# Kernel optimization log

Hardware: AMD Instinct MI355X
Metric: run time of the kernel (lower is better)

## Reference

```python
import jax, jax.numpy as jnp
import numpy as np

L_LEVELS = 10
LEVEL_DIM = 4
BASE_RES = 16
T_HASH = 2 ** 21
DEG_VIEW = 4
DENSITY_BIAS = -1.0
RGB_PADDING = 0.001
RES = (BASE_RES * 2 ** np.arange(L_LEVELS)).astype(np.float32)  # 16..8192
CORNERS = np.array([[(i >> 2) & 1, (i >> 1) & 1, i & 1] for i in range(8)], np.int32)  # [8,3]
P1 = jnp.uint32(2654435761)
P2 = jnp.uint32(805459861)


def hash_grid_encode(pts, embeddings):
    """pts [N,3] in [-1,1]; embeddings [L,T,D] -> [N,L,D] trilinear hash-grid features."""
    x01 = (pts + 1.0) * 0.5  # [N,3] in [0,1]

    def level(emb, r):
        pos = x01 * r - 0.5  # align_corners=False style
        p0 = jnp.floor(pos)
        frac = pos - p0  # [N,3]
        coords = (p0.astype(jnp.int32)[:, None, :] + CORNERS).astype(jnp.uint32)  # [N,8,3]
        h = coords[..., 0] ^ (coords[..., 1] * P1) ^ (coords[..., 2] * P2)
        idx = (h & jnp.uint32(T_HASH - 1)).astype(jnp.int32)  # [N,8]
        w = jnp.prod(jnp.where(CORNERS == 1, frac[:, None, :], 1.0 - frac[:, None, :]), axis=-1)  # [N,8]
        vals = emb[idx]  # [N,8,D]
        return jnp.einsum('ncd,nc->nd', vals, w)

    feats = jax.vmap(level)(embeddings, jnp.asarray(RES))  # [L,N,D]
    return jnp.moveaxis(feats, 0, 1)  # [N,L,D]


def pos_enc(d, min_deg=0, max_deg=DEG_VIEW):
    scales = 2.0 ** jnp.arange(min_deg, max_deg, dtype=jnp.float32)
    xb = (d[..., None, :] * scales[:, None]).reshape(*d.shape[:-1], -1)  # [...,3*deg]
    four = jnp.sin(jnp.concatenate([xb, xb + 0.5 * jnp.pi], axis=-1))
    return jnp.concatenate([d, four], axis=-1)  # [..., 3 + 6*deg] = 27


def setup_inputs() -> dict:
    key = jax.random.key(0)
    ks = jax.random.split(key, 10)
    B, S, n = 1024, 32, 6
    means = jax.random.uniform(ks[0], (B, S, n, 3), minval=-1.0, maxval=1.0)
    stds = jax.random.uniform(ks[1], (B, S, n), minval=0.001, maxval=0.05)
    vd = jax.random.normal(ks[2], (B, 3))
    viewdirs = vd / jnp.linalg.norm(vd, axis=-1, keepdims=True)
    embeddings = jax.random.normal(ks[3], (L_LEVELS, T_HASH, LEVEL_DIM)) * 0.1

    def lin(k, i, o):
        return jax.random.normal(k, (i, o)) * (1.0 / np.sqrt(i))

    return {
        'rand': 0,
        'means': means, 'stds': stds, 'viewdirs': viewdirs, 'embeddings': embeddings,
        'Wd0': lin(ks[4], 40, 64), 'bd0': jnp.zeros(64),
        'Wd1': lin(ks[5], 64, 256), 'bd1': jnp.zeros(256),
        'Wv0': lin(ks[6], 283, 256), 'bv0': jnp.zeros(256),
        'Wv1': lin(ks[7], 539, 256), 'bv1': jnp.zeros(256),
        'Wr': lin(ks[8], 256, 3), 'br': jnp.zeros(3),
    }


def reference(rand, means, stds, viewdirs, embeddings, Wd0, bd0, Wd1, bd1,
              Wv0, bv0, Wv1, bv1, Wr, br):
    B, S, n = means.shape[:3]
    # --- predict_density ---
    feats = hash_grid_encode(means.reshape(-1, 3), embeddings)
    feats = feats.reshape(B, S, n, L_LEVELS, LEVEL_DIM)
    gs = jnp.asarray(RES)
    # erf re-weighting by per-level grid size (ZipNeRF anti-aliasing)
    w = jax.lax.erf(1.0 / jnp.clip(jnp.sqrt(8.0 * stds[..., None] ** 2 * gs ** 2), 1e-10))  # [B,S,n,L]
    feat = (feats * w[..., None]).mean(axis=-3).reshape(B, S, L_LEVELS * LEVEL_DIM)  # mean over multisamples n
    h = jax.nn.relu(feat @ Wd0 + bd0)
    x = h @ Wd1 + bd1  # [B,S,256] bottleneck
    density = jax.nn.softplus(x[..., 0] + DENSITY_BIAS)
    # --- view-dependent rgb branch ---
    dir_enc = pos_enc(viewdirs)  # [B,27]
    de = jnp.broadcast_to(dir_enc[:, None, :], (B, S, dir_enc.shape[-1]))
    x_in = jnp.concatenate([x, de], axis=-1)  # [B,S,283]
    h = jax.nn.relu(x_in @ Wv0 + bv0)
    h = jnp.concatenate([h, x_in], axis=-1)  # skip connection at layer 0 -> [B,S,539]
    h = jax.nn.relu(h @ Wv1 + bv1)
    rgb = jax.nn.sigmoid(h @ Wr + br)  # rgb_premultiplier=1, rgb_bias=0
    rgb = rgb * (1.0 + 2.0 * RGB_PADDING) - RGB_PADDING
    return density, rgb
```

## Files before the change

kernel.cpp:

```cpp
#include <hip/hip_runtime.h>

#define HASH_T    2097152u
#define HASH_MASK 2097151u
#define PRIME1 2654435761u
#define PRIME2 805459861u

typedef __attribute__((ext_vector_type(8))) short bf16x8;
typedef __attribute__((ext_vector_type(4))) float f32x4;
typedef __attribute__((ext_vector_type(4))) unsigned short us4;

__device__ __forceinline__ unsigned short bf16_hi(float x){
    unsigned u = __float_as_uint(x);
    return (unsigned short)((u + 0x7FFFu + ((u >> 16) & 1u)) >> 16);
}
__device__ __forceinline__ float bf16f(unsigned short h){
    return __uint_as_float((unsigned)h << 16);
}
__device__ __forceinline__ void split2(float x, unsigned short& h, unsigned short& l){
    h = bf16_hi(x);
    l = bf16_hi(x - bf16f(h));
}

__global__ __launch_bounds__(256) void pack_weights_kernel(
    const float* __restrict__ Wd0, const float* __restrict__ Wd1,
    const float* __restrict__ Wv0, const float* __restrict__ Wv1,
    unsigned short* __restrict__ pk)
{
    int tid = blockIdx.x * 256 + threadIdx.x;
    if (tid >= 424 * 512) return;
    int pair = tid >> 9;
    int li   = tid & 511;
    int lane = li >> 3, j = li & 7;
    int kq = ((lane >> 4) << 3) + j;
    int cl = lane & 15;
    float w;
    if (pair < 8) {
        int idx = pair; int kt = idx >> 2, ct = idx & 3;
        int k = kt * 32 + kq, c = ct * 16 + cl;
        w = (k < 40) ? Wd0[k * 64 + c] : 0.0f;
    } else if (pair < 40) {
        int idx = pair - 8; int kt = idx >> 4, ct = idx & 15;
        int k = kt * 32 + kq, c = ct * 16 + cl;
        w = Wd1[k * 256 + c];
    } else if (pair < 168) {
        int idx = pair - 40; int kt = idx >> 4, ct = idx & 15;
        int k = kt * 32 + kq, c = ct * 16 + cl;
        w = Wv0[k * 256 + c];
    } else {
        int idx = pair - 168;
        int kt = idx >> 4, ct = idx & 15;
        int k = kt * 32 + kq, c = ct * 16 + cl;
        int refr = (k < 256) ? (k + 256) : (k - 256);
        w = Wv1[refr * 256 + c];
    }
    unsigned short h, l; split2(w, h, l);
    pk[(size_t)pair * 1024 + li]       = h;
    pk[(size_t)pair * 1024 + 512 + li] = l;
}

__global__ __launch_bounds__(256) void hash_encode_kernel(
    const float* __restrict__ means, const float* __restrict__ stds,
    const float* __restrict__ emb, float* __restrict__ feat, int NS)
{
    int gid = blockIdx.x * 256 + threadIdx.x;
    if (gid >= NS * 10) return;
    int l = gid / NS;
    int s = gid - l * NS;
    float r = (float)(16 << l);
    const float* __restrict__ embL = emb + (size_t)l * (size_t)HASH_T * 4u;

    float a0 = 0.f, a1 = 0.f, a2 = 0.f, a3 = 0.f;
    #pragma unroll
    for (int n = 0; n < 6; ++n) {
        const float* mp = means + ((size_t)s * 6 + n) * 3;
        float sd = stds[(size_t)s * 6 + n];
        float px = (mp[0] + 1.0f) * 0.5f * r - 0.5f;
        float py = (mp[1] + 1.0f) * 0.5f * r - 0.5f;
        float pz = (mp[2] + 1.0f) * 0.5f * r - 0.5f;
        float fx = floorf(px), fy = floorf(py), fz = floorf(pz);
        float rx = px - fx, ry = py - fy, rz = pz - fz;
        int ix = (int)fx, iy = (int)fy, iz = (int)fz;
        unsigned hx[2] = { (unsigned)ix,          (unsigned)(ix + 1) };
        unsigned hy[2] = { (unsigned)iy * PRIME1, (unsigned)(iy + 1) * PRIME1 };
        unsigned hz[2] = { (unsigned)iz * PRIME2, (unsigned)(iz + 1) * PRIME2 };
        float wx[2] = { 1.0f - rx, rx };
        float wy[2] = { 1.0f - ry, ry };
        float wz[2] = { 1.0f - rz, rz };
        float t8 = 8.0f * (sd * sd) * (r * r);
        float wl = erff(1.0f / fmaxf(sqrtf(t8), 1e-10f));
        float v0 = 0.f, v1 = 0.f, v2 = 0.f, v3 = 0.f;
        #pragma unroll
        for (int c = 0; c < 8; ++c) {
            int bx = (c >> 2) & 1, by = (c >> 1) & 1, bz = c & 1;
            unsigned idx = (hx[bx] ^ hy[by] ^ hz[bz]) & HASH_MASK;
            const float4 e = *reinterpret_cast<const float4*>(embL + (size_t)idx * 4u);
            float w = wx[bx] * wy[by] * wz[bz];
            v0 += w * e.x; v1 += w * e.y; v2 += w * e.z; v3 += w * e.w;
        }
        a0 += wl * v0; a1 += wl * v1; a2 += wl * v2; a3 += wl * v3;
    }
    const float inv6 = 1.0f / 6.0f;
    float4 o; o.x = a0 * inv6; o.y = a1 * inv6; o.z = a2 * inv6; o.w = a3 * inv6;
    *reinterpret_cast<float4*>(feat + (size_t)s * 40 + l * 4) = o;
}

template<int KT, int NC>
__device__ __forceinline__ void gemm_layer(
    const unsigned short* __restrict__ pkBase, int NCT, int ct0, int kOff,
    const unsigned short (*Ahi)[584], const unsigned short (*Alo)[584],
    int lane, f32x4 acc[NC][2])
{
    const int r = lane & 15;
    const int kg = (lane >> 4) * 8;
    for (int kt = 0; kt < KT; ++kt) {
        const int ke = kOff + kt * 32 + kg;
        bf16x8 bh[2], bl[2];
        #pragma unroll
        for (int st = 0; st < 2; ++st) {
            bh[st] = *reinterpret_cast<const bf16x8*>(&Ahi[st * 16 + r][ke]);
            bl[st] = *reinterpret_cast<const bf16x8*>(&Alo[st * 16 + r][ke]);
        }
        #pragma unroll
        for (int ci = 0; ci < NC; ++ci) {
            const unsigned short* pf = pkBase + (size_t)(kt * NCT + ct0 + ci) * 1024 + lane * 8;
            bf16x8 ah = *reinterpret_cast<const bf16x8*>(pf);
            bf16x8 al = *reinterpret_cast<const bf16x8*>(pf + 512);
            #pragma unroll
            for (int st = 0; st < 2; ++st) {
                acc[ci][st] = __builtin_amdgcn_mfma_f32_16x16x32_bf16(ah, bh[st], acc[ci][st], 0, 0, 0);
                acc[ci][st] = __builtin_amdgcn_mfma_f32_16x16x32_bf16(ah, bl[st], acc[ci][st], 0, 0, 0);
                acc[ci][st] = __builtin_amdgcn_mfma_f32_16x16x32_bf16(al, bh[st], acc[ci][st], 0, 0, 0);
            }
        }
    }
}

template<int NC, bool RELU>
__device__ __forceinline__ void epilogue_store(
    f32x4 acc[NC][2], int ct0, int lane, const float* bias, int outOff,
    unsigned short (*Ahi)[584], unsigned short (*Alo)[584])
{
    const int r = lane & 15, g = lane >> 4;
    #pragma unroll
    for (int ci = 0; ci < NC; ++ci) {
        const int c0 = (ct0 + ci) * 16 + g * 4;
        const float4 bb = *reinterpret_cast<const float4*>(&bias[c0]);
        #pragma unroll
        for (int st = 0; st < 2; ++st) {
            const int s = st * 16 + r;
            float v[4] = { acc[ci][st][0] + bb.x, acc[ci][st][1] + bb.y,
                           acc[ci][st][2] + bb.z, acc[ci][st][3] + bb.w };
            us4 H, L;
            #pragma unroll
            for (int q = 0; q < 4; ++q) {
                float vv = RELU ? fmaxf(v[q], 0.0f) : v[q];
                unsigned short h, l; split2(vv, h, l);
                H[q] = h; L[q] = l;
            }
            *reinterpret_cast<us4*>(&Ahi[s][outOff + c0]) = H;
            *reinterpret_cast<us4*>(&Alo[s][outOff + c0]) = L;
        }
    }
}

__global__ __launch_bounds__(256, 2) void mlp_mfma_kernel(
    const float* __restrict__ feat, const float* __restrict__ vdirs,
    const unsigned short* __restrict__ pk,
    const float* __restrict__ bd0, const float* __restrict__ bd1,
    const float* __restrict__ Wv0, const float* __restrict__ bv0,
    const float* __restrict__ Wv1, const float* __restrict__ bv1,
    const float* __restrict__ Wr,  const float* __restrict__ br,
    float* __restrict__ outD, float* __restrict__ outRGB)
{
    __shared__ __align__(16) unsigned short sAhi[32][584];
    __shared__ __align__(16) unsigned short sAlo[32][584];
    __shared__ float sDe[32];
    __shared__ float sDv0[256];
    __shared__ float sDv1[256];
    __shared__ float sRed[32][8][3];

    const int t = threadIdx.x;
    const int lane = t & 63;
    const int w = t >> 6;
    const int b = blockIdx.x;
    const int base = b * 32;

    {
        int s = t >> 3, kg = t & 7;
        float v[8];
        if (kg < 5) {
            const float* fp = feat + (size_t)(base + s) * 40 + kg * 8;
            #pragma unroll
            for (int q = 0; q < 8; ++q) v[q] = fp[q];
        } else {
            #pragma unroll
            for (int q = 0; q < 8; ++q) v[q] = 0.0f;
        }
        us4 H0, H1, L0v, L1v;
        #pragma unroll
        for (int q = 0; q < 4; ++q) {
            unsigned short h, l;
            split2(v[q], h, l);       H0[q] = h; L0v[q] = l;
            split2(v[q + 4], h, l);   H1[q] = h; L1v[q] = l;
        }
        *reinterpret_cast<us4*>(&sAhi[s][kg * 8])     = H0;
        *reinterpret_cast<us4*>(&sAhi[s][kg * 8 + 4]) = H1;
        *reinterpret_cast<us4*>(&sAlo[s][kg * 8])     = L0v;
        *reinterpret_cast<us4*>(&sAlo[s][kg * 8 + 4]) = L1v;
    }
    if (t < 27) {
        float d0 = vdirs[b * 3 + 0], d1 = vdirs[b * 3 + 1], d2 = vdirs[b * 3 + 2];
        float val;
        if (t < 3) val = (t == 0) ? d0 : ((t == 1) ? d1 : d2);
        else {
            int u = t - 3, half = u / 12, jk = u % 12;
            int j = jk / 3, k = jk % 3;
            float dk = (k == 0) ? d0 : ((k == 1) ? d1 : d2);
            float xb = dk * (float)(1 << j);
            val = sinf(half ? (xb + 1.57079632679489662f) : xb);
        }
        sDe[t] = val;
    }
    __syncthreads();

    {
        int c = t;
        float a0 = bv0[c], a1 = bv1[c];
        #pragma unroll
        for (int k = 0; k < 27; ++k) {
            float dv = sDe[k];
            a0 += dv * Wv0[(256 + k) * 256 + c];
            a1 += dv * Wv1[(512 + k) * 256 + c];
        }
        sDv0[c] = a0; sDv1[c] = a1;
    }

    {
        f32x4 acc[1][2] = {};
        gemm_layer<2, 1>(pk, 4, w, 0, sAhi, sAlo, lane, acc);
        __syncthreads();
        epilogue_store<1, true>(acc, w, lane, bd0, 0, sAhi, sAlo);
    }
    __syncthreads();

    {
        f32x4 acc[4][2] = {};
        gemm_layer<2, 4>(pk + 8192, 16, w * 4, 0, sAhi, sAlo, lane, acc);
        if (w == 0 && (lane >> 4) == 0) {
            #pragma unroll
            for (int st = 0; st < 2; ++st) {
                float x0 = acc[0][st][0] + bd1[0];
                int s = st * 16 + (lane & 15);
                float vv = x0 - 1.0f;
                outD[base + s] = fmaxf(vv, 0.0f) + log1pf(expf(-fabsf(vv)));
            }
        }
        epilogue_store<4, false>(acc, w * 4, lane, bd1, 64, sAhi, sAlo);
    }
    __syncthreads();

    {
        f32x4 acc[4][2] = {};
        gemm_layer<8, 4>(pk + 40960, 16, w * 4, 64, sAhi, sAlo, lane, acc);
        epilogue_store<4, true>(acc, w * 4, lane, sDv0, 320, sAhi, sAlo);
    }
    __syncthreads();

    {
        f32x4 acc[4][2] = {};
        gemm_layer<16, 4>(pk + 172032, 16, w * 4, 64, sAhi, sAlo, lane, acc);
        __syncthreads();
        epilogue_store<4, true>(acc, w * 4, lane, sDv1, 0, sAhi, sAlo);
    }
    __syncthreads();

    {
        int s = t & 31, jj = t >> 5;
        float p0 = 0.f, p1 = 0.f, p2 = 0.f;
        int k0 = jj * 32;
        #pragma unroll 2
        for (int q = 0; q < 4; ++q) {
            us4 vh[2], vl[2];
            *reinterpret_cast<uint4*>(vh) = *reinterpret_cast<const uint4*>(&sAhi[s][k0 + q * 8]);
            *reinterpret_cast<uint4*>(vl) = *reinterpret_cast<const uint4*>(&sAlo[s][k0 + q * 8]);
            #pragma unroll
            for (int e = 0; e < 8; ++e) {
                int k = k0 + q * 8 + e;
                float hv = bf16f(((const unsigned short*)vh)[e]) + bf16f(((const unsigned short*)vl)[e]);
                p0 += hv * Wr[k * 3 + 0];
                p1 += hv * Wr[k * 3 + 1];
                p2 += hv * Wr[k * 3 + 2];
            }
        }
        sRed[s][jj][0] = p0; sRed[s][jj][1] = p1; sRed[s][jj][2] = p2;
    }
    __syncthreads();
    if (t < 96) {
        int s = t & 31, ch = t >> 5;
        float a = br[ch];
        #pragma unroll
        for (int j = 0; j < 8; ++j) a += sRed[s][j][ch];
        float sg = 1.0f / (1.0f + expf(-a));
        outRGB[(size_t)(base + s) * 3 + ch] = sg * 1.002f - 0.001f;
    }
}

extern "C" void kernel_launch(void* const* d_in, const int* in_sizes, int n_in,
                              void* d_out, int out_size, void* d_ws, size_t ws_size,
                              hipStream_t stream) {
    const float* means = (const float*)d_in[1];
    const float* stds_ = (const float*)d_in[2];
    const float* vdirs = (const float*)d_in[3];
    const float* emb   = (const float*)d_in[4];
    const float* Wd0 = (const float*)d_in[5];
    const float* bd0 = (const float*)d_in[6];
    const float* Wd1 = (const float*)d_in[7];
    const float* bd1 = (const float*)d_in[8];
    const float* Wv0 = (const float*)d_in[9];
    const float* bv0 = (const float*)d_in[10];
    const float* Wv1 = (const float*)d_in[11];
    const float* bv1 = (const float*)d_in[12];
    const float* Wr  = (const float*)d_in[13];
    const float* br  = (const float*)d_in[14];

    const int B  = in_sizes[3] / 3;
    const int NS = B * 32;

    float* feat = (float*)d_ws;
    unsigned short* pk = (unsigned short*)((char*)d_ws + (size_t)NS * 40 * 4);

    hipLaunchKernelGGL(pack_weights_kernel, dim3((424 * 512 + 255) / 256), dim3(256), 0, stream,
                       Wd0, Wd1, Wv0, Wv1, pk);

    int total = NS * 10;
    hipLaunchKernelGGL(hash_encode_kernel, dim3((total + 255) / 256), dim3(256), 0, stream,
                       means, stds_, emb, feat, NS);

    float* outD   = (float*)d_out;
    float* outRGB = outD + NS;
    hipLaunchKernelGGL(mlp_mfma_kernel, dim3(B), dim3(256), 0, stream,
                       feat, vdirs, pk, bd0, bd1, Wv0, bv0, Wv1, bv1, Wr, br,
                       outD, outRGB);
}
```

Measured before the change: 229.9 us.

## Fuse hash-grid encoding into MLP kernel and shrink LDS activation buffer

Moves the hash-grid encode into the MLP kernel: 8 threads per sample gather embeddings per level, and xor-shuffles reduce over the multisamples. This removes the intermediate feature buffer and one kernel launch. The second view layer's K loop is split so its skip-input half is computed early. That lets the LDS row stride shrink from 584 to 328 and occupancy rise to 3 blocks. Weight fragments are prefetched one K-tile ahead and the RGB reduction uses shuffles. In exchange, gather latency is now exposed inside the MLP kernel and more barriers are added.

```diff
diff --git a/kernel.cpp b/kernel.cpp
--- a/kernel.cpp
+++ b/kernel.cpp
@@ -8,6 +8,8 @@
 typedef __attribute__((ext_vector_type(8))) short bf16x8;
 typedef __attribute__((ext_vector_type(4))) float f32x4;
 typedef __attribute__((ext_vector_type(4))) unsigned short us4;
+
+#define LDS_STRIDE 328
 
 __device__ __forceinline__ unsigned short bf16_hi(float x){
     unsigned u = __float_as_uint(x);
@@ -58,61 +60,33 @@
     pk[(size_t)pair * 1024 + 512 + li] = l;
 }
 
-__global__ __launch_bounds__(256) void hash_encode_kernel(
-    const float* __restrict__ means, const float* __restrict__ stds,
-    const float* __restrict__ emb, float* __restrict__ feat, int NS)
-{
-    int gid = blockIdx.x * 256 + threadIdx.x;
-    if (gid >= NS * 10) return;
-    int l = gid / NS;
-    int s = gid - l * NS;
-    float r = (float)(16 << l);
-    const float* __restrict__ embL = emb + (size_t)l * (size_t)HASH_T * 4u;
-
-    float a0 = 0.f, a1 = 0.f, a2 = 0.f, a3 = 0.f;
-    #pragma unroll
-    for (int n = 0; n < 6; ++n) {
-        const float* mp = means + ((size_t)s * 6 + n) * 3;
-        float sd = stds[(size_t)s * 6 + n];
-        float px = (mp[0] + 1.0f) * 0.5f * r - 0.5f;
-        float py = (mp[1] + 1.0f) * 0.5f * r - 0.5f;
-        float pz = (mp[2] + 1.0f) * 0.5f * r - 0.5f;
-        float fx = floorf(px), fy = floorf(py), fz = floorf(pz);
-        float rx = px - fx, ry = py - fy, rz = pz - fz;
-        int ix = (int)fx, iy = (int)fy, iz = (int)fz;
-        unsigned hx[2] = { (unsigned)ix,          (unsigned)(ix + 1) };
-        unsigned hy[2] = { (unsigned)iy * PRIME1, (unsigned)(iy + 1) * PRIME1 };
-        unsigned hz[2] = { (unsigned)iz * PRIME2, (unsigned)(iz + 1) * PRIME2 };
-        float wx[2] = { 1.0f - rx, rx };
-        float wy[2] = { 1.0f - ry, ry };
-        float wz[2] = { 1.0f - rz, rz };
-        float t8 = 8.0f * (sd * sd) * (r * r);
-        float wl = erff(1.0f / fmaxf(sqrtf(t8), 1e-10f));
-        float v0 = 0.f, v1 = 0.f, v2 = 0.f, v3 = 0.f;
-        #pragma unroll
-        for (int c = 0; c < 8; ++c) {
-            int bx = (c >> 2) & 1, by = (c >> 1) & 1, bz = c & 1;
-            unsigned idx = (hx[bx] ^ hy[by] ^ hz[bz]) & HASH_MASK;
-            const float4 e = *reinterpret_cast<const float4*>(embL + (size_t)idx * 4u);
-            float w = wx[bx] * wy[by] * wz[bz];
-            v0 += w * e.x; v1 += w * e.y; v2 += w * e.z; v3 += w * e.w;
-        }
-        a0 += wl * v0; a1 += wl * v1; a2 += wl * v2; a3 += wl * v3;
-    }
-    const float inv6 = 1.0f / 6.0f;
-    float4 o; o.x = a0 * inv6; o.y = a1 * inv6; o.z = a2 * inv6; o.w = a3 * inv6;
-    *reinterpret_cast<float4*>(feat + (size_t)s * 40 + l * 4) = o;
-}
-
 template<int KT, int NC>
-__device__ __forceinline__ void gemm_layer(
+__device__ __forceinline__ void gemm32(
     const unsigned short* __restrict__ pkBase, int NCT, int ct0, int kOff,
-    const unsigned short (*Ahi)[584], const unsigned short (*Alo)[584],
+    const unsigned short (*Ahi)[LDS_STRIDE], const unsigned short (*Alo)[LDS_STRIDE],
     int lane, f32x4 acc[NC][2])
 {
     const int r = lane & 15;
     const int kg = (lane >> 4) * 8;
+    bf16x8 ah[NC], al[NC];
+    #pragma unroll
+    for (int ci = 0; ci < NC; ++ci) {
+        const unsigned short* pf = pkBase + (size_t)(ct0 + ci) * 1024 + (size_t)lane * 8;
+        ah[ci] = *reinterpret_cast<const bf16x8*>(pf);
+        al[ci] = *reinterpret_cast<const bf16x8*>(pf + 512);
+    }
+    #pragma unroll
     for (int kt = 0; kt < KT; ++kt) {
+        bf16x8 ahn[NC], aln[NC];
+        if (kt + 1 < KT) {
+            #pragma unroll
+            for (int ci = 0; ci < NC; ++ci) {
+                const unsigned short* pf = pkBase
+                    + (size_t)((kt + 1) * NCT + ct0 + ci) * 1024 + (size_t)lane * 8;
+                ahn[ci] = *reinterpret_cast<const bf16x8*>(pf);
+                aln[ci] = *reinterpret_cast<const bf16x8*>(pf + 512);
+            }
+        }
         const int ke = kOff + kt * 32 + kg;
         bf16x8 bh[2], bl[2];
         #pragma unroll
@@ -122,23 +96,24 @@
         }
         #pragma unroll
         for (int ci = 0; ci < NC; ++ci) {
-            const unsigned short* pf = pkBase + (size_t)(kt * NCT + ct0 + ci) * 1024 + lane * 8;
-            bf16x8 ah = *reinterpret_cast<const bf16x8*>(pf);
-            bf16x8 al = *reinterpret_cast<const bf16x8*>(pf + 512);
             #pragma unroll
             for (int st = 0; st < 2; ++st) {
-                acc[ci][st] = __builtin_amdgcn_mfma_f32_16x16x32_bf16(ah, bh[st], acc[ci][st], 0, 0, 0);
-                acc[ci][st] = __builtin_amdgcn_mfma_f32_16x16x32_bf16(ah, bl[st], acc[ci][st], 0, 0, 0);
-                acc[ci][st] = __builtin_amdgcn_mfma_f32_16x16x32_bf16(al, bh[st], acc[ci][st], 0, 0, 0);
-            }
+                acc[ci][st] = __builtin_amdgcn_mfma_f32_16x16x32_bf16(ah[ci], bh[st], acc[ci][st], 0, 0, 0);
+                acc[ci][st] = __builtin_amdgcn_mfma_f32_16x16x32_bf16(ah[ci], bl[st], acc[ci][st], 0, 0, 0);
+                acc[ci][st] = __builtin_amdgcn_mfma_f32_16x16x32_bf16(al[ci], bh[st], acc[ci][st], 0, 0, 0);
+            }
+        }
+        if (kt + 1 < KT) {
+            #pragma unroll
+            for (int ci = 0; ci < NC; ++ci) { ah[ci] = ahn[ci]; al[ci] = aln[ci]; }
         }
     }
 }
 
 template<int NC, bool RELU>
-__device__ __forceinline__ void epilogue_store(
+__device__ __forceinline__ void epi32(
     f32x4 acc[NC][2], int ct0, int lane, const float* bias, int outOff,
-    unsigned short (*Ahi)[584], unsigned short (*Alo)[584])
+    unsigned short (*Ahi)[LDS_STRIDE], unsigned short (*Alo)[LDS_STRIDE])
 {
     const int r = lane & 15, g = lane >> 4;
     #pragma unroll
@@ -163,8 +138,9 @@
     }
 }
 
-__global__ __launch_bounds__(256, 2) void mlp_mfma_kernel(
-    const float* __restrict__ feat, const float* __restrict__ vdirs,
+__global__ __launch_bounds__(256, 3) void zip_fused_kernel(
+    const float* __restrict__ means, const float* __restrict__ stds,
+    const float* __restrict__ vdirs, const float* __restrict__ emb,
     const unsigned short* __restrict__ pk,
     const float* __restrict__ bd0, const float* __restrict__ bd1,
     const float* __restrict__ Wv0, const float* __restrict__ bv0,
@@ -172,12 +148,11 @@
     const float* __restrict__ Wr,  const float* __restrict__ br,
     float* __restrict__ outD, float* __restrict__ outRGB)
 {
-    __shared__ __align__(16) unsigned short sAhi[32][584];
-    __shared__ __align__(16) unsigned short sAlo[32][584];
+    __shared__ __align__(16) unsigned short sAhi[32][LDS_STRIDE];
+    __shared__ __align__(16) unsigned short sAlo[32][LDS_STRIDE];
     __shared__ float sDe[32];
     __shared__ float sDv0[256];
     __shared__ float sDv1[256];
-    __shared__ float sRed[32][8][3];
 
     const int t = threadIdx.x;
     const int lane = t & 63;
@@ -185,28 +160,11 @@
     const int b = blockIdx.x;
     const int base = b * 32;
 
-    {
-        int s = t >> 3, kg = t & 7;
-        float v[8];
-        if (kg < 5) {
-            const float* fp = feat + (size_t)(base + s) * 40 + kg * 8;
-            #pragma unroll
-            for (int q = 0; q < 8; ++q) v[q] = fp[q];
-        } else {
-            #pragma unroll
-            for (int q = 0; q < 8; ++q) v[q] = 0.0f;
-        }
-        us4 H0, H1, L0v, L1v;
-        #pragma unroll
-        for (int q = 0; q < 4; ++q) {
-            unsigned short h, l;
-            split2(v[q], h, l);       H0[q] = h; L0v[q] = l;
-            split2(v[q + 4], h, l);   H1[q] = h; L1v[q] = l;
-        }
-        *reinterpret_cast<us4*>(&sAhi[s][kg * 8])     = H0;
-        *reinterpret_cast<us4*>(&sAhi[s][kg * 8 + 4]) = H1;
-        *reinterpret_cast<us4*>(&sAlo[s][kg * 8])     = L0v;
-        *reinterpret_cast<us4*>(&sAlo[s][kg * 8 + 4]) = L1v;
+    if (t < 192) {
+        int s = t / 6, j = t - s * 6;
+        us4 z = {0, 0, 0, 0};
+        *reinterpret_cast<us4*>(&sAhi[s][40 + j * 4]) = z;
+        *reinterpret_cast<us4*>(&sAlo[s][40 + j * 4]) = z;
     }
     if (t < 27) {
         float d0 = vdirs[b * 3 + 0], d1 = vdirs[b * 3 + 1], d2 = vdirs[b * 3 + 2];
@@ -224,9 +182,71 @@
     __syncthreads();
 
     {
+        const int s = t >> 3, n = t & 7;
+        const bool act = (n < 6);
+        float mx = 0.f, my = 0.f, mz = 0.f, sd2_8 = 0.f;
+        if (act) {
+            const float* mp = means + ((size_t)(base + s) * 6 + n) * 3;
+            mx = mp[0]; my = mp[1]; mz = mp[2];
+            float sd = stds[(size_t)(base + s) * 6 + n];
+            sd2_8 = 8.0f * sd * sd;
+        }
+        const float inv6 = 1.0f / 6.0f;
+        #pragma unroll 2
+        for (int l = 0; l < 10; ++l) {
+            float r = (float)(16 << l);
+            float a0 = 0.f, a1 = 0.f, a2 = 0.f, a3 = 0.f;
+            if (act) {
+                float px = (mx + 1.0f) * 0.5f * r - 0.5f;
+                float py = (my + 1.0f) * 0.5f * r - 0.5f;
+                float pz = (mz + 1.0f) * 0.5f * r - 0.5f;
+                float fx = floorf(px), fy = floorf(py), fz = floorf(pz);
+                float rx = px - fx, ry = py - fy, rz = pz - fz;
+                int ix = (int)fx, iy = (int)fy, iz = (int)fz;
+                unsigned hx[2] = { (unsigned)ix,          (unsigned)(ix + 1) };
+                unsigned hy[2] = { (unsigned)iy * PRIME1, (unsigned)(iy + 1) * PRIME1 };
+                unsigned hz[2] = { (unsigned)iz * PRIME2, (unsigned)(iz + 1) * PRIME2 };
+                float wx[2] = { 1.0f - rx, rx };
+                float wy[2] = { 1.0f - ry, ry };
+                float wz[2] = { 1.0f - rz, rz };
+                float wl = erff(1.0f / fmaxf(sqrtf(sd2_8 * r * r), 1e-10f));
+                #pragma unroll
+                for (int c = 0; c < 8; ++c) {
+                    int cx = (c >> 2) & 1, cy = (c >> 1) & 1, cz = c & 1;
+                    unsigned idx = (hx[cx] ^ hy[cy] ^ hz[cz]) & HASH_MASK;
+                    const float4 e = *reinterpret_cast<const float4*>(
+                        emb + ((size_t)l * HASH_T + idx) * 4u);
+                    float wgt = wx[cx] * wy[cy] * wz[cz];
+                    a0 += wgt * e.x; a1 += wgt * e.y; a2 += wgt * e.z; a3 += wgt * e.w;
+                }
+                a0 *= wl; a1 *= wl; a2 *= wl; a3 *= wl;
+            }
+            #pragma unroll
+            for (int m = 1; m < 8; m <<= 1) {
+                a0 += __shfl_xor(a0, m);
+                a1 += __shfl_xor(a1, m);
+                a2 += __shfl_xor(a2, m);
+                a3 += __shfl_xor(a3, m);
+            }
+            if (n == 0) {
+                float o[4] = { a0 * inv6, a1 * inv6, a2 * inv6, a3 * inv6 };
+                us4 H, L;
+                #pragma unroll
+                for (int q = 0; q < 4; ++q) {
+                    unsigned short h, lo; split2(o[q], h, lo);
+                    H[q] = h; L[q] = lo;
+                }
+                *reinterpret_cast<us4*>(&sAhi[s][l * 4]) = H;
+                *reinterpret_cast<us4*>(&sAlo[s][l * 4]) = L;
+            }
+        }
+    }
+    __syncthreads();
+
+    {
         int c = t;
         float a0 = bv0[c], a1 = bv1[c];
-        #pragma unroll
+        #pragma unroll 3
         for (int k = 0; k < 27; ++k) {
             float dv = sDe[k];
             a0 += dv * Wv0[(256 + k) * 256 + c];
@@ -234,18 +254,19 @@
         }
         sDv0[c] = a0; sDv1[c] = a1;
     }
+    __syncthreads();
 
     {
         f32x4 acc[1][2] = {};
-        gemm_layer<2, 1>(pk, 4, w, 0, sAhi, sAlo, lane, acc);
+        gemm32<2, 1>(pk, 4, w, 0, sAhi, sAlo, lane, acc);
         __syncthreads();
-        epilogue_store<1, true>(acc, w, lane, bd0, 0, sAhi, sAlo);
+        epi32<1, true>(acc, w, lane, bd0, 0, sAhi, sAlo);
     }
     __syncthreads();
 
     {
         f32x4 acc[4][2] = {};
-        gemm_layer<2, 4>(pk + 8192, 16, w * 4, 0, sAhi, sAlo, lane, acc);
+        gemm32<2, 4>(pk + 8192, 16, w * 4, 0, sAhi, sAlo, lane, acc);
         if (w == 0 && (lane >> 4) == 0) {
             #pragma unroll
             for (int st = 0; st < 2; ++st) {
@@ -255,29 +276,33 @@
                 outD[base + s] = fmaxf(vv, 0.0f) + log1pf(expf(-fabsf(vv)));
             }
         }
-        epilogue_store<4, false>(acc, w * 4, lane, bd1, 64, sAhi, sAlo);
-    }
+        __syncthreads();
+        epi32<4, false>(acc, w * 4, lane, bd1, 64, sAhi, sAlo);
+    }
+    __syncthreads();
+
+    f32x4 px[4][2] = {};
+    gemm32<8, 4>(pk + 172032, 16, w * 4, 64, sAhi, sAlo, lane, px);
     __syncthreads();
 
     {
         f32x4 acc[4][2] = {};
-        gemm_layer<8, 4>(pk + 40960, 16, w * 4, 64, sAhi, sAlo, lane, acc);
-        epilogue_store<4, true>(acc, w * 4, lane, sDv0, 320, sAhi, sAlo);
-    }
-    __syncthreads();
-
-    {
-        f32x4 acc[4][2] = {};
-        gemm_layer<16, 4>(pk + 172032, 16, w * 4, 64, sAhi, sAlo, lane, acc);
+        gemm32<8, 4>(pk + 40960, 16, w * 4, 64, sAhi, sAlo, lane, acc);
         __syncthreads();
-        epilogue_store<4, true>(acc, w * 4, lane, sDv1, 0, sAhi, sAlo);
-    }
-    __syncthreads();
-
-    {
-        int s = t & 31, jj = t >> 5;
+        epi32<4, true>(acc, w * 4, lane, sDv0, 64, sAhi, sAlo);
+    }
+    __syncthreads();
+
+    {
+        gemm32<8, 4>(pk + 303104, 16, w * 4, 64, sAhi, sAlo, lane, px);
+        __syncthreads();
+        epi32<4, true>(px, w * 4, lane, sDv1, 64, sAhi, sAlo);
+    }
+    __syncthreads();
+
+    {
+        int s = t >> 3, j = t & 7, k0 = 64 + j * 32;
         float p0 = 0.f, p1 = 0.f, p2 = 0.f;
-        int k0 = jj * 32;
         #pragma unroll 2
         for (int q = 0; q < 4; ++q) {
             us4 vh[2], vl[2];
@@ -285,23 +310,24 @@
             *reinterpret_cast<uint4*>(vl) = *reinterpret_cast<const uint4*>(&sAlo[s][k0 + q * 8]);
             #pragma unroll
             for (int e = 0; e < 8; ++e) {
-                int k = k0 + q * 8 + e;
+                int k = j * 32 + q * 8 + e;
                 float hv = bf16f(((const unsigned short*)vh)[e]) + bf16f(((const unsigned short*)vl)[e]);
                 p0 += hv * Wr[k * 3 + 0];
                 p1 += hv * Wr[k * 3 + 1];
                 p2 += hv * Wr[k * 3 + 2];
             }
         }
-        sRed[s][jj][0] = p0; sRed[s][jj][1] = p1; sRed[s][jj][2] = p2;
-    }
-    __syncthreads();
-    if (t < 96) {
-        int s = t & 31, ch = t >> 5;
-        float a = br[ch];
         #pragma unroll
-        for (int j = 0; j < 8; ++j) a += sRed[s][j][ch];
-        float sg = 1.0f / (1.0f + expf(-a));
-        outRGB[(size_t)(base + s) * 3 + ch] = sg * 1.002f - 0.001f;
+        for (int m = 1; m < 8; m <<= 1) {
+            p0 += __shfl_xor(p0, m);
+            p1 += __shfl_xor(p1, m);
+            p2 += __shfl_xor(p2, m);
+        }
+        if (j < 3) {
+            float a = ((j == 0) ? p0 : (j == 1) ? p1 : p2) + br[j];
+            float sg = 1.0f / (1.0f + expf(-a));
+            outRGB[(size_t)(base + s) * 3 + j] = sg * 1.002f - 0.001f;
+        }
     }
 }
 
@@ -326,19 +352,15 @@
     const int B  = in_sizes[3] / 3;
     const int NS = B * 32;
 
-    float* feat = (float*)d_ws;
-    unsigned short* pk = (unsigned short*)((char*)d_ws + (size_t)NS * 40 * 4);
+    unsigned short* pk = (unsigned short*)d_ws;
 
     hipLaunchKernelGGL(pack_weights_kernel, dim3((424 * 512 + 255) / 256), dim3(256), 0, stream,
                        Wd0, Wd1, Wv0, Wv1, pk);
 
-    int total = NS * 10;
-    hipLaunchKernelGGL(hash_encode_kernel, dim3((total + 255) / 256), dim3(256), 0, stream,
-                       means, stds_, emb, feat, NS);
-
     float* outD   = (float*)d_out;
     float* outRGB = outD + NS;
-    hipLaunchKernelGGL(mlp_mfma_kernel, dim3(B), dim3(256), 0, stream,
-                       feat, vdirs, pk, bd0, bd1, Wv0, bv0, Wv1, bv1, Wr, br,
+    hipLaunchKernelGGL(zip_fused_kernel, dim3(B), dim3(256), 0, stream,
+                       means, stds_, vdirs, emb, pk,
+                       bd0, bd1, Wv0, bv0, Wv1, bv1, Wr, br,
                        outD, outRGB);
 }
```

New measurement: 191.4 us. -16.7%, faster.

## Shrink MLP LDS footprint by splitting skip-layer GEMM and raise occupancy

Applied to the files above, without the earlier changes.

Reduces the shared activation buffers from 584 to 328 columns by splitting the second view-layer GEMM into two K-halves. The x_in half is accumulated into a register accumulator before the first view layer overwrites the skip region, and the second half runs after it. Launch bounds go from 2 to 3 blocks per CU, weight fragments are prefetched one k-tile ahead in registers, and the RGB reduction uses wave shuffles instead of an LDS buffer. The cost is extra barriers and more live registers, since the split accumulator stays live across a whole GEMM, which may cause spills at the tighter register budget.

```diff
diff --git a/kernel.cpp b/kernel.cpp
--- a/kernel.cpp
+++ b/kernel.cpp
@@ -8,6 +8,8 @@
 typedef __attribute__((ext_vector_type(8))) short bf16x8;
 typedef __attribute__((ext_vector_type(4))) float f32x4;
 typedef __attribute__((ext_vector_type(4))) unsigned short us4;
+
+#define LDS_STRIDE 328
 
 __device__ __forceinline__ unsigned short bf16_hi(float x){
     unsigned u = __float_as_uint(x);
@@ -105,14 +107,32 @@
 }
 
 template<int KT, int NC>
-__device__ __forceinline__ void gemm_layer(
+__device__ __forceinline__ void gemm32(
     const unsigned short* __restrict__ pkBase, int NCT, int ct0, int kOff,
-    const unsigned short (*Ahi)[584], const unsigned short (*Alo)[584],
+    const unsigned short (*Ahi)[LDS_STRIDE], const unsigned short (*Alo)[LDS_STRIDE],
     int lane, f32x4 acc[NC][2])
 {
     const int r = lane & 15;
     const int kg = (lane >> 4) * 8;
+    bf16x8 ah[NC], al[NC];
+    #pragma unroll
+    for (int ci = 0; ci < NC; ++ci) {
+        const unsigned short* pf = pkBase + (size_t)(ct0 + ci) * 1024 + (size_t)lane * 8;
+        ah[ci] = *reinterpret_cast<const bf16x8*>(pf);
+        al[ci] = *reinterpret_cast<const bf16x8*>(pf + 512);
+    }
+    #pragma unroll
     for (int kt = 0; kt < KT; ++kt) {
+        bf16x8 ahn[NC], aln[NC];
+        if (kt + 1 < KT) {
+            #pragma unroll
+            for (int ci = 0; ci < NC; ++ci) {
+                const unsigned short* pf = pkBase
+                    + (size_t)((kt + 1) * NCT + ct0 + ci) * 1024 + (size_t)lane * 8;
+                ahn[ci] = *reinterpret_cast<const bf16x8*>(pf);
+                aln[ci] = *reinterpret_cast<const bf16x8*>(pf + 512);
+            }
+        }
         const int ke = kOff + kt * 32 + kg;
         bf16x8 bh[2], bl[2];
         #pragma unroll
@@ -122,23 +142,24 @@
         }
         #pragma unroll
         for (int ci = 0; ci < NC; ++ci) {
-            const unsigned short* pf = pkBase + (size_t)(kt * NCT + ct0 + ci) * 1024 + lane * 8;
-            bf16x8 ah = *reinterpret_cast<const bf16x8*>(pf);
-            bf16x8 al = *reinterpret_cast<const bf16x8*>(pf + 512);
             #pragma unroll
             for (int st = 0; st < 2; ++st) {
-                acc[ci][st] = __builtin_amdgcn_mfma_f32_16x16x32_bf16(ah, bh[st], acc[ci][st], 0, 0, 0);
-                acc[ci][st] = __builtin_amdgcn_mfma_f32_16x16x32_bf16(ah, bl[st], acc[ci][st], 0, 0, 0);
-                acc[ci][st] = __builtin_amdgcn_mfma_f32_16x16x32_bf16(al, bh[st], acc[ci][st], 0, 0, 0);
-            }
+                acc[ci][st] = __builtin_amdgcn_mfma_f32_16x16x32_bf16(ah[ci], bh[st], acc[ci][st], 0, 0, 0);
+                acc[ci][st] = __builtin_amdgcn_mfma_f32_16x16x32_bf16(ah[ci], bl[st], acc[ci][st], 0, 0, 0);
+                acc[ci][st] = __builtin_amdgcn_mfma_f32_16x16x32_bf16(al[ci], bh[st], acc[ci][st], 0, 0, 0);
+            }
+        }
+        if (kt + 1 < KT) {
+            #pragma unroll
+            for (int ci = 0; ci < NC; ++ci) { ah[ci] = ahn[ci]; al[ci] = aln[ci]; }
         }
     }
 }
 
 template<int NC, bool RELU>
-__device__ __forceinline__ void epilogue_store(
+__device__ __forceinline__ void epi32(
     f32x4 acc[NC][2], int ct0, int lane, const float* bias, int outOff,
-    unsigned short (*Ahi)[584], unsigned short (*Alo)[584])
+    unsigned short (*Ahi)[LDS_STRIDE], unsigned short (*Alo)[LDS_STRIDE])
 {
     const int r = lane & 15, g = lane >> 4;
     #pragma unroll
@@ -163,7 +184,7 @@
     }
 }
 
-__global__ __launch_bounds__(256, 2) void mlp_mfma_kernel(
+__global__ __launch_bounds__(256, 3) void mlp_mfma_kernel(
     const float* __restrict__ feat, const float* __restrict__ vdirs,
     const unsigned short* __restrict__ pk,
     const float* __restrict__ bd0, const float* __restrict__ bd1,
@@ -172,12 +193,11 @@
     const float* __restrict__ Wr,  const float* __restrict__ br,
     float* __restrict__ outD, float* __restrict__ outRGB)
 {
-    __shared__ __align__(16) unsigned short sAhi[32][584];
-    __shared__ __align__(16) unsigned short sAlo[32][584];
+    __shared__ __align__(16) unsigned short sAhi[32][LDS_STRIDE];
+    __shared__ __align__(16) unsigned short sAlo[32][LDS_STRIDE];
     __shared__ float sDe[32];
     __shared__ float sDv0[256];
     __shared__ float sDv1[256];
-    __shared__ float sRed[32][8][3];
 
     const int t = threadIdx.x;
     const int lane = t & 63;
@@ -189,9 +209,10 @@
         int s = t >> 3, kg = t & 7;
         float v[8];
         if (kg < 5) {
-            const float* fp = feat + (size_t)(base + s) * 40 + kg * 8;
-            #pragma unroll
-            for (int q = 0; q < 8; ++q) v[q] = fp[q];
+            const float4 f0 = *reinterpret_cast<const float4*>(feat + (size_t)(base + s) * 40 + kg * 8);
+            const float4 f1 = *reinterpret_cast<const float4*>(feat + (size_t)(base + s) * 40 + kg * 8 + 4);
+            v[0]=f0.x; v[1]=f0.y; v[2]=f0.z; v[3]=f0.w;
+            v[4]=f1.x; v[5]=f1.y; v[6]=f1.z; v[7]=f1.w;
         } else {
             #pragma unroll
             for (int q = 0; q < 8; ++q) v[q] = 0.0f;
@@ -226,7 +247,7 @@
     {
         int c = t;
         float a0 = bv0[c], a1 = bv1[c];
-        #pragma unroll
+        #pragma unroll 3
         for (int k = 0; k < 27; ++k) {
             float dv = sDe[k];
             a0 += dv * Wv0[(256 + k) * 256 + c];
@@ -234,18 +255,19 @@
         }
         sDv0[c] = a0; sDv1[c] = a1;
     }
+    __syncthreads();
 
     {
         f32x4 acc[1][2] = {};
-        gemm_layer<2, 1>(pk, 4, w, 0, sAhi, sAlo, lane, acc);
+        gemm32<2, 1>(pk, 4, w, 0, sAhi, sAlo, lane, acc);
         __syncthreads();
-        epilogue_store<1, true>(acc, w, lane, bd0, 0, sAhi, sAlo);
+        epi32<1, true>(acc, w, lane, bd0, 0, sAhi, sAlo);
     }
     __syncthreads();
 
     {
         f32x4 acc[4][2] = {};
-        gemm_layer<2, 4>(pk + 8192, 16, w * 4, 0, sAhi, sAlo, lane, acc);
+        gemm32<2, 4>(pk + 8192, 16, w * 4, 0, sAhi, sAlo, lane, acc);
         if (w == 0 && (lane >> 4) == 0) {
             #pragma unroll
             for (int st = 0; st < 2; ++st) {
@@ -255,29 +277,33 @@
                 outD[base + s] = fmaxf(vv, 0.0f) + log1pf(expf(-fabsf(vv)));
             }
         }
-        epilogue_store<4, false>(acc, w * 4, lane, bd1, 64, sAhi, sAlo);
-    }
+        __syncthreads();
+        epi32<4, false>(acc, w * 4, lane, bd1, 64, sAhi, sAlo);
+    }
+    __syncthreads();
+
+    f32x4 px[4][2] = {};
+    gemm32<8, 4>(pk + 172032, 16, w * 4, 64, sAhi, sAlo, lane, px);
     __syncthreads();
 
     {
         f32x4 acc[4][2] = {};
-        gemm_layer<8, 4>(pk + 40960, 16, w * 4, 64, sAhi, sAlo, lane, acc);
-        epilogue_store<4, true>(acc, w * 4, lane, sDv0, 320, sAhi, sAlo);
-    }
-    __syncthreads();
-
-    {
-        f32x4 acc[4][2] = {};
-        gemm_layer<16, 4>(pk + 172032, 16, w * 4, 64, sAhi, sAlo, lane, acc);
+        gemm32<8, 4>(pk + 40960, 16, w * 4, 64, sAhi, sAlo, lane, acc);
         __syncthreads();
-        epilogue_store<4, true>(acc, w * 4, lane, sDv1, 0, sAhi, sAlo);
-    }
-    __syncthreads();
-
-    {
-        int s = t & 31, jj = t >> 5;
+        epi32<4, true>(acc, w * 4, lane, sDv0, 64, sAhi, sAlo);
+    }
+    __syncthreads();
+
+    {
+        gemm32<8, 4>(pk + 303104, 16, w * 4, 64, sAhi, sAlo, lane, px);
+        __syncthreads();
+        epi32<4, true>(px, w * 4, lane, sDv1, 64, sAhi, sAlo);
+    }
+    __syncthreads();
+
+    {
+        int s = t >> 3, j = t & 7, k0 = 64 + j * 32;
         float p0 = 0.f, p1 = 0.f, p2 = 0.f;
-        int k0 = jj * 32;
         #pragma unroll 2
         for (int q = 0; q < 4; ++q) {
             us4 vh[2], vl[2];
@@ -285,23 +311,24 @@
             *reinterpret_cast<uint4*>(vl) = *reinterpret_cast<const uint4*>(&sAlo[s][k0 + q * 8]);
             #pragma unroll
             for (int e = 0; e < 8; ++e) {
-                int k = k0 + q * 8 + e;
+                int k = j * 32 + q * 8 + e;
                 float hv = bf16f(((const unsigned short*)vh)[e]) + bf16f(((const unsigned short*)vl)[e]);
                 p0 += hv * Wr[k * 3 + 0];
                 p1 += hv * Wr[k * 3 + 1];
                 p2 += hv * Wr[k * 3 + 2];
             }
         }
-        sRed[s][jj][0] = p0; sRed[s][jj][1] = p1; sRed[s][jj][2] = p2;
-    }
-    __syncthreads();
-    if (t < 96) {
-        int s = t & 31, ch = t >> 5;
-        float a = br[ch];
-        #pragma unroll
-        for (int j = 0; j < 8; ++j) a += sRed[s][j][ch];
-        float sg = 1.0f / (1.0f + expf(-a));
-        outRGB[(size_t)(base + s) * 3 + ch] = sg * 1.002f - 0.001f;
+        #pragma unroll
+        for (int m = 1; m < 8; m <<= 1) {
+            p0 += __shfl_xor(p0, m);
+            p1 += __shfl_xor(p1, m);
+            p2 += __shfl_xor(p2, m);
+        }
+        if (j < 3) {
+            float a = ((j == 0) ? p0 : (j == 1) ? p1 : p2) + br[j];
+            float sg = 1.0f / (1.0f + expf(-a));
+            outRGB[(size_t)(base + s) * 3 + j] = sg * 1.002f - 0.001f;
+        }
     }
 }
 
```

New measurement: 224.0 us. 2.5% less time.
